# Kernel optimization log

Hardware: AMD Instinct MI355X
Metric: run time of the kernel (lower is better)

## Reference

```python
import jax, jax.numpy as jnp
import numpy as np

B, L, D = 4, 8192, 512


def setup_inputs() -> dict:
    key = jax.random.key(0)
    kx, kwg, kwc = jax.random.split(key, 3)
    x = jax.random.normal(kx, (B, L, D), dtype=jnp.float32)
    # Xavier-uniform init for DxD linears
    bound = float(np.sqrt(6.0 / (D + D)))
    Wg = jax.random.uniform(kwg, (D, D), minval=-bound, maxval=bound, dtype=jnp.float32)
    bg = jnp.ones((D,), dtype=jnp.float32)   # gate bias init to 1.0
    Wc = jax.random.uniform(kwc, (D, D), minval=-bound, maxval=bound, dtype=jnp.float32)
    bc = jnp.zeros((D,), dtype=jnp.float32)
    return {"x": x, "Wg": Wg, "bg": bg, "Wc": Wc, "bc": bc}


def _mingru_scan(gates, cands):
    # h_t = (1 - g_t) * h_{t-1} + g_t * c_t, h_0 = 0
    # linear recurrence h_t = a_t h_{t-1} + b_t with a = 1-g, b = g*c
    a = 1.0 - gates
    b = gates * cands

    def combine(left, right):
        a_l, b_l = left
        a_r, b_r = right
        return a_r * a_l, a_r * b_l + b_r

    _, h = jax.lax.associative_scan(combine, (a, b), axis=1)
    return h


def reference(x, Wg, bg, Wc, bc):
    gates = jax.nn.sigmoid(jnp.einsum('bld,ed->ble', x, Wg) + bg)
    cands = jnp.tanh(jnp.einsum('bld,ed->ble', x, Wc) + bc)
    return _mingru_scan(gates, cands)
```

## Files before the change

kernel.cpp:

```cpp
#include <hip/hip_runtime.h>
#include <stdint.h>
#include <stddef.h>

#define B_ 4
#define L_ 8192
#define D_ 512
#define M_ (B_*L_)
#define K_ 512
#define CHUNK 64
#define NC (L_/CHUNK)

typedef _Float16 f16;
typedef f16 f16x2 __attribute__((ext_vector_type(2)));
typedef f16 f16x4 __attribute__((ext_vector_type(4)));
typedef f16 f16x8 __attribute__((ext_vector_type(8)));
typedef float f32x4 __attribute__((ext_vector_type(4)));

__device__ __forceinline__ void async16(const void* g, void* l) {
  __builtin_amdgcn_global_load_lds(
      (const __attribute__((address_space(1))) uint32_t*)g,
      (__attribute__((address_space(3))) uint32_t*)l,
      16, 0, 0);
}

__global__ __launch_bounds__(256) void prep(const float* __restrict__ x,
                                            const float* __restrict__ Wg,
                                            const float* __restrict__ Wc,
                                            f16* __restrict__ xh,
                                            f16* __restrict__ wp) {
  const int bid = blockIdx.x;
  if (bid < 16384) {
    const int idx = (bid * 256 + threadIdx.x) * 4;
    float4 v = *(const float4*)(x + idx);
    f16x4 o = {(f16)v.x, (f16)v.y, (f16)v.z, (f16)v.w};
    *(f16x4*)(xh + idx) = o;
  } else {
    const int idx = ((bid - 16384) * 256 + threadIdx.x) * 4;
    const float* src = (idx < 262144) ? (Wg + idx) : (Wc + (idx - 262144));
    float4 v = *(const float4*)src;
    f16x4 o = {(f16)v.x, (f16)v.y, (f16)v.z, (f16)v.w};
    *(f16x4*)(wp + idx) = o;
  }
}

__global__ __launch_bounds__(512, 2) void gemm_act(
    const f16* __restrict__ Xh, const f16* __restrict__ Wp,
    const float* __restrict__ bg, const float* __restrict__ bc,
    uint32_t* __restrict__ AC,
    float* __restrict__ cA, float* __restrict__ cB) {
  __shared__ __align__(16) f16 sA[2][256 * 32];
  __shared__ __align__(16) f16 sBg[2][128 * 32];
  __shared__ __align__(16) f16 sBc[2][128 * 32];

  const int tid = threadIdx.x;
  const int id = blockIdx.x;
  const int xcd = id & 7;
  const int slot = id >> 3;
  const int g_ = xcd * 64 + slot;
  const int bm = g_ >> 2;
  const int bn = g_ & 3;

  const int lane = tid & 63;
  const int w = tid >> 6;
  const int wm = w >> 1, wn = w & 1;
  const int l15 = lane & 15, quad = lane >> 4;

  const int srow = tid >> 2;
  const int spc8 = (tid & 3) * 8;
  const f16* gA  = Xh + (size_t)(bm * 256 + srow) * K_ + spc8;
  const f16* gBg = Wp + (size_t)(bn * 128 + srow) * K_ + spc8;
  const f16* gBc = Wp + (size_t)(512 + bn * 128 + srow) * K_ + spc8;

  f32x4 accG[4][4] = {};
  f32x4 accC[4][4] = {};

#define STAGE(kk, b) { \
    async16(gA + (kk),  &sA[b][tid * 8]); \
    async16(gA + (size_t)128 * K_ + (kk), &sA[b][tid * 8 + 128 * 32]); \
    async16(gBg + (kk), &sBg[b][tid * 8]); \
    async16(gBc + (kk), &sBc[b][tid * 8]); }

#define COMPUTE(bC) { \
    f16x8 af[4], bgf[4], bcf[4]; \
    _Pragma("unroll") \
    for (int i = 0; i < 4; i++) \
      af[i] = *(const f16x8*)(&sA[bC][(wm * 64 + i * 16 + l15) * 32 + quad * 8]); \
    _Pragma("unroll") \
    for (int j = 0; j < 4; j++) { \
      bgf[j] = *(const f16x8*)(&sBg[bC][(wn * 64 + j * 16 + l15) * 32 + quad * 8]); \
      bcf[j] = *(const f16x8*)(&sBc[bC][(wn * 64 + j * 16 + l15) * 32 + quad * 8]); \
    } \
    _Pragma("unroll") \
    for (int i = 0; i < 4; i++) \
      _Pragma("unroll") \
      for (int j = 0; j < 4; j++) { \
        accG[i][j] = __builtin_amdgcn_mfma_f32_16x16x32_f16(af[i], bgf[j], accG[i][j], 0, 0, 0); \
        accC[i][j] = __builtin_amdgcn_mfma_f32_16x16x32_f16(af[i], bcf[j], accC[i][j], 0, 0, 0); \
      } }

  STAGE(0, 0);
  asm volatile("s_waitcnt vmcnt(0)" ::: "memory");
  __builtin_amdgcn_s_barrier();

#pragma unroll
  for (int t = 0; t < 15; t++) {
    const int c = t & 1, n = c ^ 1;
    STAGE((t + 1) * 32, n);
    COMPUTE(c);
    asm volatile("s_waitcnt vmcnt(0)" ::: "memory");
    __builtin_amdgcn_s_barrier();
  }
  COMPUTE(1);
#undef COMPUTE
#undef STAGE

  const int c = bm * 4 + wm;
#pragma unroll
  for (int j = 0; j < 4; j++) {
    const int col = bn * 128 + wn * 64 + j * 16 + l15;
    const float bgv = bg[col];
    const float bcv = bc[col];
    float blkP[4], blkQ[4];
#pragma unroll
    for (int i = 0; i < 4; i++) {
      const int mrow = bm * 256 + wm * 64 + i * 16 + quad * 4;
      float P = 1.0f, Q = 0.0f;
#pragma unroll
      for (int r = 0; r < 4; r++) {
        float yg = accG[i][j][r] + bgv;
        float gg = 1.0f / (1.0f + __expf(-yg));
        float yc = accC[i][j][r] + bcv;
        yc = fminf(fmaxf(yc, -15.0f), 15.0f);
        float t = __expf(2.0f * yc);
        float cc = (t - 1.0f) / (t + 1.0f);
        f16x2 p;
        p[0] = (f16)(1.0f - gg);
        p[1] = (f16)(gg * cc);
        *(f16x2*)&AC[(size_t)(mrow + r) * 512 + col] = p;
        const float av = (float)p[0];
        const float bv = (float)p[1];
        Q = fmaf(av, Q, bv);
        P *= av;
      }
      float Pp = __shfl_xor(P, 16);
      float Qp = __shfl_xor(Q, 16);
      float nP = P * Pp;
      float nQ = (quad & 1) ? fmaf(P, Qp, Q) : fmaf(Pp, Q, Qp);
      Pp = __shfl_xor(nP, 32);
      Qp = __shfl_xor(nQ, 32);
      blkP[i] = nP * Pp;
      blkQ[i] = (quad & 2) ? fmaf(nP, Qp, nQ) : fmaf(Pp, nQ, Qp);
    }
    float CP = blkP[0], CQ = blkQ[0];
#pragma unroll
    for (int i = 1; i < 4; i++) {
      CQ = fmaf(blkP[i], CQ, blkQ[i]);
      CP *= blkP[i];
    }
    if (quad == 0) {
      cA[(size_t)c * 512 + col] = CP;
      cB[(size_t)c * 512 + col] = CQ;
    }
  }
}

__global__ __launch_bounds__(128) void scan_apply(
    const uint32_t* __restrict__ AC,
    const float* __restrict__ cA, const float* __restrict__ cB,
    float* __restrict__ out) {
  const int blk = blockIdx.x;
  const int ch = blk & (NC - 1);
  const int bseq = blk >> 7;
  const int d0 = threadIdx.x * 4;

  float h0 = 0.0f, h1 = 0.0f, h2 = 0.0f, h3 = 0.0f;
  const float* pA = cA + (size_t)(bseq * NC) * 512 + d0;
  const float* pB = cB + (size_t)(bseq * NC) * 512 + d0;
#pragma unroll 4
  for (int cc = 0; cc < ch; cc++) {
    float4 va = *(const float4*)(pA + (size_t)cc * 512);
    float4 vb = *(const float4*)(pB + (size_t)cc * 512);
    h0 = fmaf(va.x, h0, vb.x);
    h1 = fmaf(va.y, h1, vb.y);
    h2 = fmaf(va.z, h2, vb.z);
    h3 = fmaf(va.w, h3, vb.w);
  }

  const size_t base = (size_t)blk * CHUNK * 512 + d0;
#pragma unroll 8
  for (int t = 0; t < CHUNK; t++) {
    const size_t i = base + (size_t)t * 512;
    uint4 v = *(const uint4*)&AC[i];
    f16x2 p0 = __builtin_bit_cast(f16x2, v.x);
    f16x2 p1 = __builtin_bit_cast(f16x2, v.y);
    f16x2 p2 = __builtin_bit_cast(f16x2, v.z);
    f16x2 p3 = __builtin_bit_cast(f16x2, v.w);
    h0 = fmaf((float)p0[0], h0, (float)p0[1]);
    h1 = fmaf((float)p1[0], h1, (float)p1[1]);
    h2 = fmaf((float)p2[0], h2, (float)p2[1]);
    h3 = fmaf((float)p3[0], h3, (float)p3[1]);
    float4 o;
    o.x = h0; o.y = h1; o.z = h2; o.w = h3;
    *(float4*)&out[i] = o;
  }
}

extern "C" void kernel_launch(void* const* d_in, const int* in_sizes, int n_in,
                              void* d_out, int out_size, void* d_ws, size_t ws_size,
                              hipStream_t stream) {
  const float* x  = (const float*)d_in[0];
  const float* Wg = (const float*)d_in[1];
  const float* bg = (const float*)d_in[2];
  const float* Wc = (const float*)d_in[3];
  const float* bc = (const float*)d_in[4];
  float* out = (float*)d_out;

  char* ws = (char*)d_ws;
  f16*      xh = (f16*)(ws);
  f16*      wp = (f16*)(ws + 33554432);
  uint32_t* AC = (uint32_t*)(ws + 34603008);
  float*    cA = (float*)(ws + 101711872);
  float*    cB = (float*)(ws + 102760448);

  prep<<<16896, 256, 0, stream>>>(x, Wg, Wc, xh, wp);
  gemm_act<<<512, 512, 0, stream>>>(xh, wp, bg, bc, AC, cA, cB);
  scan_apply<<<B_ * NC, 128, 0, stream>>>(AC, cA, cB, out);
}
```

Measured before the change: 206.0 us.

## Swizzle fp16 operands in prep and double GEMM K-tile to 64

```diff
diff --git a/kernel.cpp b/kernel.cpp
--- a/kernel.cpp
+++ b/kernel.cpp
@@ -29,18 +29,23 @@
                                             f16* __restrict__ xh,
                                             f16* __restrict__ wp) {
   const int bid = blockIdx.x;
-  if (bid < 16384) {
-    const int idx = (bid * 256 + threadIdx.x) * 4;
-    float4 v = *(const float4*)(x + idx);
-    f16x4 o = {(f16)v.x, (f16)v.y, (f16)v.z, (f16)v.w};
-    *(f16x4*)(xh + idx) = o;
-  } else {
-    const int idx = ((bid - 16384) * 256 + threadIdx.x) * 4;
-    const float* src = (idx < 262144) ? (Wg + idx) : (Wc + (idx - 262144));
-    float4 v = *(const float4*)src;
-    f16x4 o = {(f16)v.x, (f16)v.y, (f16)v.z, (f16)v.w};
-    *(f16x4*)(wp + idx) = o;
-  }
+  const int isX = (bid < 8192);
+  const int U = (isX ? bid : (bid - 8192)) * 256 + threadIdx.x;
+  const int r  = U >> 6;
+  const int w_ = U & 63;
+  const int s  = w_ >> 3;
+  const int u3 = w_ & 7;
+  const int du = (r << 6) + (s << 3) + (u3 ^ (r & 7));
+  const float* src;
+  if (isX)            src = x + (size_t)U * 8;
+  else if (r < 512)   src = Wg + (size_t)r * 512 + w_ * 8;
+  else                src = Wc + (size_t)(r - 512) * 512 + w_ * 8;
+  float4 v0 = *(const float4*)src;
+  float4 v1 = *(const float4*)(src + 4);
+  f16x8 o = {(f16)v0.x, (f16)v0.y, (f16)v0.z, (f16)v0.w,
+             (f16)v1.x, (f16)v1.y, (f16)v1.z, (f16)v1.w};
+  f16* dst = isX ? xh : wp;
+  *(f16x8*)(dst + (size_t)du * 8) = o;
 }
 
 __global__ __launch_bounds__(512, 2) void gemm_act(
@@ -48,9 +53,9 @@
     const float* __restrict__ bg, const float* __restrict__ bc,
     uint32_t* __restrict__ AC,
     float* __restrict__ cA, float* __restrict__ cB) {
-  __shared__ __align__(16) f16 sA[2][256 * 32];
-  __shared__ __align__(16) f16 sBg[2][128 * 32];
-  __shared__ __align__(16) f16 sBc[2][128 * 32];
+  __shared__ __align__(16) f16 sA[2][256 * 64];
+  __shared__ __align__(16) f16 sBg[2][128 * 64];
+  __shared__ __align__(16) f16 sBc[2][128 * 64];
 
   const int tid = threadIdx.x;
   const int id = blockIdx.x;
@@ -65,47 +70,58 @@
   const int wm = w >> 1, wn = w & 1;
   const int l15 = lane & 15, quad = lane >> 4;
 
-  const int srow = tid >> 2;
-  const int spc8 = (tid & 3) * 8;
-  const f16* gA  = Xh + (size_t)(bm * 256 + srow) * K_ + spc8;
-  const f16* gBg = Wp + (size_t)(bn * 128 + srow) * K_ + spc8;
-  const f16* gBc = Wp + (size_t)(512 + bn * 128 + srow) * K_ + spc8;
+  const int srow = tid >> 3;
+  const int sp8 = (tid & 7) * 8;
+  const f16* gA  = Xh + (size_t)(bm * 256 + srow) * K_ + sp8;
+  const f16* gBg = Wp + (size_t)(bn * 128 + srow) * K_ + sp8;
+  const f16* gBc = Wp + (size_t)(512 + bn * 128 + srow) * K_ + sp8;
+
+  const int xu0 = (quad ^ (l15 & 7)) * 8;
+  const int xu1 = xu0 ^ 32;
 
   f32x4 accG[4][4] = {};
   f32x4 accC[4][4] = {};
 
 #define STAGE(kk, b) { \
-    async16(gA + (kk),  &sA[b][tid * 8]); \
-    async16(gA + (size_t)128 * K_ + (kk), &sA[b][tid * 8 + 128 * 32]); \
-    async16(gBg + (kk), &sBg[b][tid * 8]); \
-    async16(gBc + (kk), &sBc[b][tid * 8]); }
+    async16(gA + (kk),                    &sA[b][tid * 8]); \
+    async16(gA + (size_t) 64 * K_ + (kk), &sA[b][tid * 8 +  64 * 64]); \
+    async16(gA + (size_t)128 * K_ + (kk), &sA[b][tid * 8 + 128 * 64]); \
+    async16(gA + (size_t)192 * K_ + (kk), &sA[b][tid * 8 + 192 * 64]); \
+    async16(gBg + (kk),                   &sBg[b][tid * 8]); \
+    async16(gBg + (size_t)64 * K_ + (kk), &sBg[b][tid * 8 + 64 * 64]); \
+    async16(gBc + (kk),                   &sBc[b][tid * 8]); \
+    async16(gBc + (size_t)64 * K_ + (kk), &sBc[b][tid * 8 + 64 * 64]); }
 
 #define COMPUTE(bC) { \
-    f16x8 af[4], bgf[4], bcf[4]; \
     _Pragma("unroll") \
-    for (int i = 0; i < 4; i++) \
-      af[i] = *(const f16x8*)(&sA[bC][(wm * 64 + i * 16 + l15) * 32 + quad * 8]); \
-    _Pragma("unroll") \
-    for (int j = 0; j < 4; j++) { \
-      bgf[j] = *(const f16x8*)(&sBg[bC][(wn * 64 + j * 16 + l15) * 32 + quad * 8]); \
-      bcf[j] = *(const f16x8*)(&sBc[bC][(wn * 64 + j * 16 + l15) * 32 + quad * 8]); \
-    } \
-    _Pragma("unroll") \
-    for (int i = 0; i < 4; i++) \
+    for (int k32 = 0; k32 < 2; k32++) { \
+      const int xu = k32 ? xu1 : xu0; \
+      f16x8 af[4], bgf[4], bcf[4]; \
+      _Pragma("unroll") \
+      for (int i = 0; i < 4; i++) \
+        af[i] = *(const f16x8*)(&sA[bC][(wm * 64 + i * 16 + l15) * 64 + xu]); \
       _Pragma("unroll") \
       for (int j = 0; j < 4; j++) { \
-        accG[i][j] = __builtin_amdgcn_mfma_f32_16x16x32_f16(af[i], bgf[j], accG[i][j], 0, 0, 0); \
-        accC[i][j] = __builtin_amdgcn_mfma_f32_16x16x32_f16(af[i], bcf[j], accC[i][j], 0, 0, 0); \
-      } }
+        bgf[j] = *(const f16x8*)(&sBg[bC][(wn * 64 + j * 16 + l15) * 64 + xu]); \
+        bcf[j] = *(const f16x8*)(&sBc[bC][(wn * 64 + j * 16 + l15) * 64 + xu]); \
+      } \
+      _Pragma("unroll") \
+      for (int i = 0; i < 4; i++) \
+        _Pragma("unroll") \
+        for (int j = 0; j < 4; j++) { \
+          accG[i][j] = __builtin_amdgcn_mfma_f32_16x16x32_f16(af[i], bgf[j], accG[i][j], 0, 0, 0); \
+          accC[i][j] = __builtin_amdgcn_mfma_f32_16x16x32_f16(af[i], bcf[j], accC[i][j], 0, 0, 0); \
+        } \
+    } }
 
   STAGE(0, 0);
   asm volatile("s_waitcnt vmcnt(0)" ::: "memory");
   __builtin_amdgcn_s_barrier();
 
 #pragma unroll
-  for (int t = 0; t < 15; t++) {
+  for (int t = 0; t < 7; t++) {
     const int c = t & 1, n = c ^ 1;
-    STAGE((t + 1) * 32, n);
+    STAGE((t + 1) * 64, n);
     COMPUTE(c);
     asm volatile("s_waitcnt vmcnt(0)" ::: "memory");
     __builtin_amdgcn_s_barrier();
@@ -222,7 +238,7 @@
   float*    cA = (float*)(ws + 101711872);
   float*    cB = (float*)(ws + 102760448);
 
-  prep<<<16896, 256, 0, stream>>>(x, Wg, Wc, xh, wp);
+  prep<<<8448, 256, 0, stream>>>(x, Wg, Wc, xh, wp);
   gemm_act<<<512, 512, 0, stream>>>(xh, wp, bg, bc, AC, cA, cB);
   scan_apply<<<B_ * NC, 128, 0, stream>>>(AC, cA, cB, out);
 }
```

Measured after the change: 228.3 us. 1.11x slower.
